# Optimization experiments

Measured on AMD Instinct MI355X. Metric: run time of the kernel, lower is better.

The kernel has to match this reference:

```python
import jax, jax.numpy as jnp
import numpy as np

D = 1024
H = 16
DH = D // H
L = 128  # max_pos_len
B = 4
T = 1024
SCALE = float(np.sqrt(D / H))


def setup_inputs() -> dict:
    key = jax.random.key(0)
    ks = jax.random.split(key, 9)
    x_q = jax.random.normal(ks[0], (B, T, D), dtype=jnp.float32)
    x_k = jax.random.normal(ks[1], (B, T, D), dtype=jnp.float32)
    x_v = jax.random.normal(ks[2], (B, T, D), dtype=jnp.float32)
    mask = jax.random.randint(ks[3], (B, 1, 1, T), 0, 2) == 1  # bool, True = masked
    Wq = jax.random.normal(ks[4], (D, D), dtype=jnp.float32) * 0.02
    Wk = jax.random.normal(ks[5], (D, D), dtype=jnp.float32) * 0.02
    Wv = jax.random.normal(ks[6], (D, D), dtype=jnp.float32) * 0.02
    Wo = jax.random.normal(ks[7], (D, D), dtype=jnp.float32) * 0.02
    pos_emb = jax.random.normal(ks[8], (2 * L + 1, DH), dtype=jnp.float32)
    return {"x_q": x_q, "x_k": x_k, "x_v": x_v, "mask": mask,
            "Wq": Wq, "Wk": Wk, "Wv": Wv, "Wo": Wo, "pos_emb": pos_emb}


def reference(x_q, x_k, x_v, mask, Wq, Wk, Wv, Wo, pos_emb):
    # nn.Linear(bias=False): y = x @ W.T
    def split_heads(x):  # (B,T,D) -> (B,H,T,DH)
        return x.reshape(B, -1, H, DH).transpose(0, 2, 1, 3)

    Q = split_heads(x_q @ Wq.T)
    K = split_heads(x_k @ Wk.T)
    V = split_heads(x_v @ Wv.T)

    logits = jnp.einsum('bhqd,bhkd->bhqk', Q, K)

    # arrange_char_pos_embedding: indices[q,k] = clamp(k-q, -L, L) + L
    rel = jnp.clip(jnp.arange(T)[None, :] - jnp.arange(T)[:, None], -L, L) + L
    arranged_pos = pos_emb[rel]  # (T_Q, T_K, DH)
    pos_logits = jnp.einsum('bhqd,qkd->bhqk', Q, arranged_pos)

    logits = (logits + pos_logits) / SCALE
    logits = jnp.where(mask, -jnp.inf, logits)  # mask broadcasts (B,1,1,T)
    attn = jax.nn.softmax(logits, axis=-1)  # dropout p=0.0 -> identity

    combined = jnp.einsum('bhqk,bhkd->bhqd', attn, V)
    heads_concat = combined.transpose(0, 2, 1, 3).reshape(B, -1, D)
    return heads_concat @ Wo.T
```

## Files before the change

kernel.cpp:

```cpp
#include <hip/hip_runtime.h>
#include <hip/hip_bf16.h>
#include <stdint.h>

typedef __attribute__((ext_vector_type(8))) short short8;
typedef __attribute__((ext_vector_type(4))) float f32x4;

__device__ __forceinline__ uint16_t f2bf(float f) {
    union { float f; uint32_t u; } v; v.f = f;
    uint32_t r = v.u + 0x7FFF + ((v.u >> 16) & 1);
    return (uint16_t)(r >> 16);
}
__device__ __forceinline__ float bf2f(uint16_t u) {
    union { uint32_t u; float f; } v; v.u = ((uint32_t)u) << 16;
    return v.f;
}
__device__ __forceinline__ float exp2_raw(float x) {
    float r;
    asm("v_exp_f32 %0, %1" : "=v"(r) : "v"(x));
    return r;
}
__device__ __forceinline__ uint32_t cvt_pk_bf16(float lo, float hi) {
    uint32_t r;
    asm("v_cvt_pk_bf16_f32 %0, %1, %2" : "=v"(r) : "v"(lo), "v"(hi));
    return r;
}

template<int F32>
__device__ __forceinline__ uint4 load8(const void* p, size_t off) {
    if (F32) {
        const float* f = (const float*)p + off;
        float4 f0 = *(const float4*)f;
        float4 f1 = *(const float4*)(f + 4);
        uint4 r;
        r.x = (uint32_t)f2bf(f0.x) | ((uint32_t)f2bf(f0.y) << 16);
        r.y = (uint32_t)f2bf(f0.z) | ((uint32_t)f2bf(f0.w) << 16);
        r.z = (uint32_t)f2bf(f1.x) | ((uint32_t)f2bf(f1.y) << 16);
        r.w = (uint32_t)f2bf(f1.z) | ((uint32_t)f2bf(f1.w) << 16);
        return r;
    } else {
        return *(const uint4*)((const uint16_t*)p + off);
    }
}

#define GLDS(gp, lp) __builtin_amdgcn_global_load_lds( \
    (const __attribute__((address_space(1))) void*)(gp), \
    (__attribute__((address_space(3))) void*)(lp), 16, 0, 0)

struct CvtSeg { const float* s; uint16_t* d; int n8; };
struct CvtArgs {
    CvtSeg seg[9]; int nseg;
    const void* mraw; unsigned long long* mbits; uint16_t* mvals;
};

__global__ __launch_bounds__(256) void cvt_bf16(CvtArgs a)
{
    if (blockIdx.x == 0) {
        __shared__ int flags[3];
        __shared__ uint8_t mloc[4096];
        const uint32_t* w = (const uint32_t*)a.mraw;
        const uint8_t* b8 = (const uint8_t*)a.mraw;
        const int t = threadIdx.x;
        if (t < 3) flags[t] = 0;
        __syncthreads();
        int fbyte = 0, ff32 = 0, fodd = 0;
        for (int i = t; i < 1024; i += 256) {
            uint32_t v = w[i];
            if (v != 0u && v != 1u && v != 0x3F800000u) fbyte = 1;
            if (v == 0x3F800000u) ff32 = 1;
            if ((i & 1) && v != 0u) fodd = 1;
        }
        if (fbyte) atomicOr(&flags[0], 1);
        if (ff32)  atomicOr(&flags[1], 1);
        if (fodd)  atomicOr(&flags[2], 1);
        __syncthreads();
        int mode;
        if (flags[0]) mode = 1;
        else if (flags[1]) mode = 0;
        else if (!flags[2]) mode = 2;
        else mode = 0;
        for (int k = t; k < 4096; k += 256) {
            int val;
            if (mode == 1)      val = (b8[k] != 0);
            else if (mode == 2) val = (w[2 * k] != 0u);
            else                val = (w[k] != 0u);
            mloc[k] = (uint8_t)val;
        }
        __syncthreads();
        for (int k = t; k < 4096; k += 256)
            a.mvals[k] = mloc[k] ? (uint16_t)0 : (uint16_t)0x3F80;
        if (t < 64) {
            uint64_t bits = 0;
#pragma unroll
            for (int i = 0; i < 64; ++i)
                bits |= (uint64_t)mloc[t * 64 + i] << i;
            a.mbits[t] = bits;
        }
    }
    const int tid = blockIdx.x * 256 + threadIdx.x;
    const int stride = gridDim.x * 256;
    for (int s = 0; s < a.nseg; ++s) {
        const float* src = a.seg[s].s;
        uint16_t* dst = a.seg[s].d;
        const int n8 = a.seg[s].n8;
        if (src) {
            for (int i = tid; i < n8; i += stride)
                *(uint4*)(dst + (size_t)i * 8) = load8<1>(src, (size_t)i * 8);
        } else {
            const uint4 z = {0u, 0u, 0u, 0u};
            for (int i = tid; i < n8; i += stride)
                *(uint4*)(dst + (size_t)i * 8) = z;
        }
    }
}

__global__ __launch_bounds__(256) void gemm128_qkv(
    const uint16_t* __restrict__ xq, const uint16_t* __restrict__ xk, const uint16_t* __restrict__ xv,
    const uint16_t* __restrict__ Wq, const uint16_t* __restrict__ Wk, const uint16_t* __restrict__ Wv,
    uint16_t* __restrict__ Qh, uint16_t* __restrict__ Khd, uint16_t* __restrict__ Vt,
    const unsigned long long* __restrict__ mbits)
{
    __shared__ alignas(16) uint16_t As[2][128 * 32];
    __shared__ alignas(16) uint16_t Bs[2][128 * 32];

    const int z = blockIdx.z;
    const uint16_t* A = (z == 0) ? xq : (z == 1) ? xk : xv;
    const uint16_t* B = (z == 0) ? Wq : (z == 1) ? Wk : Wv;
    uint16_t* C = (z == 0) ? Qh : (z == 1) ? Khd : Vt;
    const int cm = (z == 2) ? 2 : 1;
    const int bm = blockIdx.x, bn = blockIdx.y;
    const int K = 1024;

    const int t = threadIdx.x;
    const int lane = t & 63, wave = t >> 6;
    const int lrow = lane & 15, quad = lane >> 4;
    const int wr = (wave >> 1) * 64, wc = (wave & 1) * 64;
    const int g_row = wave * 16 + (lane >> 2);
    const int g_col = (lane & 3) * 8;

    const f32x4 fz = {0.f, 0.f, 0.f, 0.f};
    f32x4 acc[4][4];
#pragma unroll
    for (int i = 0; i < 4; ++i)
#pragma unroll
        for (int j = 0; j < 4; ++j) acc[i][j] = fz;

    for (int k0 = 0; k0 < K; k0 += 64) {
        __syncthreads();
#pragma unroll
        for (int kh = 0; kh < 2; ++kh) {
            const int kk = k0 + kh * 32;
            GLDS(A + (size_t)(bm * 128 + g_row) * K + kk + g_col,      As[kh] + wave * 512);
            GLDS(A + (size_t)(bm * 128 + g_row + 64) * K + kk + g_col, As[kh] + wave * 512 + 2048);
            GLDS(B + (size_t)(bn * 128 + g_row) * K + kk + g_col,      Bs[kh] + wave * 512);
            GLDS(B + (size_t)(bn * 128 + g_row + 64) * K + kk + g_col, Bs[kh] + wave * 512 + 2048);
        }
        __syncthreads();

#pragma unroll
        for (int kh = 0; kh < 2; ++kh) {
            short8 a[4], b[4];
#pragma unroll
            for (int i = 0; i < 4; ++i)
                a[i] = *(const short8*)(As[kh] + (wr + i * 16 + lrow) * 32 + quad * 8);
#pragma unroll
            for (int j = 0; j < 4; ++j)
                b[j] = *(const short8*)(Bs[kh] + (wc + j * 16 + lrow) * 32 + quad * 8);
#pragma unroll
            for (int i = 0; i < 4; ++i)
#pragma unroll
                for (int j = 0; j < 4; ++j)
                    acc[i][j] = __builtin_amdgcn_mfma_f32_16x16x32_bf16(a[i], b[j], acc[i][j], 0, 0, 0);
        }
    }

    if (cm == 2) {
        __syncthreads();
        uint16_t* scr = As[0] + wave * 1024;
        const int mg0 = bm * 128 + wr;
        const int widx = __builtin_amdgcn_readfirstlane((mg0 >> 10) * 16 + ((mg0 & 1023) >> 6));
        const uint64_t mword = mbits[widx];
        const uint64_t mw64 = mword >> ((lane & 1) * 8);
#pragma unroll
        for (int i = 0; i < 4; ++i)
#pragma unroll
            for (int j = 0; j < 4; ++j) {
                uint2 pk;
                pk.x = (uint32_t)f2bf(acc[i][j][0]) | ((uint32_t)f2bf(acc[i][j][1]) << 16);
                pk.y = (uint32_t)f2bf(acc[i][j][2]) | ((uint32_t)f2bf(acc[i][j][3]) << 16);
                *(uint2*)(scr + lrow * 16 + quad * 4) = pk;
                if (lane < 32) {
                    int n = lane >> 1, m8 = (lane & 1) * 8;
                    short8 vv = *(const short8*)(scr + n * 16 + m8);
                    int ng = bn * 128 + wc + j * 16 + n;
                    int hh = ng >> 6, d = ng & 63;
                    int mg = bm * 128 + wr + i * 16;
                    int bb = mg >> 10, tl = (mg & 1023) + m8;
                    uint32_t eb = (uint32_t)(mw64 >> (i * 16)) & 0xFFu;
                    if (eb) {
                        union { short8 s; uint32_t u[4]; } uw;
                        uw.s = vv;
#pragma unroll
                        for (int c = 0; c < 4; ++c) {
                            uint32_t km = (((eb >> (2 * c)) & 1) ? 0u : 0x0000FFFFu)
                                        | (((eb >> (2 * c + 1)) & 1) ? 0u : 0xFFFF0000u);
                            uw.u[c] &= km;
                        }
                        vv = uw.s;
                    }
                    *(short8*)(C + ((((size_t)bb * 16 + hh) * 64 + d) * 1024 + tl)) = vv;
                }
            }
        return;
    }

#pragma unroll
    for (int i = 0; i < 4; ++i)
#pragma unroll
        for (int j = 0; j < 4; ++j)
#pragma unroll
            for (int r = 0; r < 4; ++r) {
                int m = bm * 128 + wr + i * 16 + quad * 4 + r;
                int n = bn * 128 + wc + j * 16 + lrow;
                int bb = m >> 10, tt = m & 1023, hh = n >> 6, d = n & 63;
                C[(((size_t)bb * 16 + hh) * 1024 + tt) * 64 + d] = f2bf(acc[i][j][r]);
            }
}

__global__ __launch_bounds__(256) void gemm_out(
    const uint16_t* __restrict__ A, const uint16_t* __restrict__ B,
    float* __restrict__ C, int M, int N, int K)
{
    __shared__ alignas(16) uint16_t As[2][64 * 32];
    __shared__ alignas(16) uint16_t Bs[2][128 * 32];

    const int t = threadIdx.x;
    const int lane = t & 63, wave = t >> 6;
    const int lrow = lane & 15, quad = lane >> 4;
    const int wr = (wave >> 1) * 32, wc = (wave & 1) * 64;
    const int g_row = wave * 16 + (lane >> 2);
    const int g_col = (lane & 3) * 8;
    const int bm = blockIdx.x, bn = blockIdx.y;

    const f32x4 fz = {0.f, 0.f, 0.f, 0.f};
    f32x4 acc[2][4];
#pragma unroll
    for (int i = 0; i < 2; ++i)
#pragma unroll
        for (int j = 0; j < 4; ++j) acc[i][j] = fz;

    for (int k0 = 0; k0 < K; k0 += 64) {
        __syncthreads();
#pragma unroll
        for (int kh = 0; kh < 2; ++kh) {
            const int kk = k0 + kh * 32;
            GLDS(A + (size_t)(bm * 64 + g_row) * K + kk + g_col,       As[kh] + wave * 512);
            GLDS(B + (size_t)(bn * 128 + g_row) * K + kk + g_col,      Bs[kh] + wave * 512);
            GLDS(B + (size_t)(bn * 128 + g_row + 64) * K + kk + g_col, Bs[kh] + wave * 512 + 2048);
        }
        __syncthreads();

#pragma unroll
        for (int kh = 0; kh < 2; ++kh) {
            short8 a[2], b[4];
#pragma unroll
            for (int i = 0; i < 2; ++i)
                a[i] = *(const short8*)(As[kh] + (wr + i * 16 + lrow) * 32 + quad * 8);
#pragma unroll
            for (int j = 0; j < 4; ++j)
                b[j] = *(const short8*)(Bs[kh] + (wc + j * 16 + lrow) * 32 + quad * 8);
#pragma unroll
            for (int i = 0; i < 2; ++i)
#pragma unroll
                for (int j = 0; j < 4; ++j)
                    acc[i][j] = __builtin_amdgcn_mfma_f32_16x16x32_bf16(a[i], b[j], acc[i][j], 0, 0, 0);
        }
    }

#pragma unroll
    for (int i = 0; i < 2; ++i)
#pragma unroll
        for (int j = 0; j < 4; ++j)
#pragma unroll
            for (int r = 0; r < 4; ++r) {
                int m = bm * 64 + wr + i * 16 + quad * 4 + r;
                int n = bn * 128 + wc + j * 16 + lrow;
                C[(size_t)m * N + n] = acc[i][j][r];
            }
}

#define FA_QK(KC_)                                                              \
{                                                                               \
    _Pragma("unroll")                                                           \
    for (int j = 0; j < 4; ++j) {                                               \
        short8 k0 = *(const short8*)((KC_) + (j * 16 + lrow) * 32 + rdc);       \
        short8 k1 = *(const short8*)((KC_) + 2048 + (j * 16 + lrow) * 32 + rdc);\
        s[j] = __builtin_amdgcn_mfma_f32_16x16x32_bf16(aq0, k0, fz, 0, 0, 0);   \
        s[j] = __builtin_amdgcn_mfma_f32_16x16x32_bf16(aq1, k1, s[j], 0, 0, 0); \
    }                                                                           \
}

#define FA_PV(KBM_)                                                             \
{                                                                               \
    short8 bm0 = *(const short8*)(maskl + (KBM_) + quad * 8);                   \
    short8 bm1 = *(const short8*)(maskl + (KBM_) + 32 + quad * 8);              \
    _Pragma("unroll")                                                           \
    for (int dt = 0; dt < 4; ++dt) {                                            \
        o[dt] = __builtin_amdgcn_mfma_f32_16x16x32_bf16(ap0, vv[dt * 2 + 0], o[dt], 0, 0, 0); \
        o[dt] = __builtin_amdgcn_mfma_f32_16x16x32_bf16(ap1, vv[dt * 2 + 1], o[dt], 0, 0, 0); \
    }                                                                           \
    lacc = __builtin_amdgcn_mfma_f32_16x16x32_bf16(ap0, bm0, lacc, 0, 0, 0);    \
    lacc = __builtin_amdgcn_mfma_f32_16x16x32_bf16(ap1, bm1, lacc, 0, 0, 0);    \
}

#define FA_SM(KB_)                                                              \
{                                                                               \
    const int diff = (KB_) - qb;                                                \
    if (diff <= -192 || diff >= 144) {                                          \
        const bool low = (diff <= -192);                                        \
        _Pragma("unroll")                                                       \
        for (int j = 0; j < 4; ++j) {                                           \
            float e[4];                                                         \
            _Pragma("unroll")                                                   \
            for (int r = 0; r < 4; ++r) {                                       \
                float pc = low ? pcl[r] : pch[r];                               \
                e[r] = exp2_raw(__builtin_fmaf(s[j][r], CS, pc));               \
            }                                                                   \
            const uint32_t p01 = cvt_pk_bf16(e[0], e[1]);                       \
            const uint32_t p23 = cvt_pk_bf16(e[2], e[3]);                       \
            const int col = j * 16 + lrow;                                      \
            const int rw = quad * 4;                                            \
            Pl[wave][rw + 0][col] = (uint16_t)p01;                              \
            Pl[wave][rw + 1][col] = (uint16_t)(p01 >> 16);                      \
            Pl[wave][rw + 2][col] = (uint16_t)p23;                              \
            Pl[wave][rw + 3][col] = (uint16_t)(p23 >> 16);                      \
        }                                                                       \
    } else {                                                                    \
        _Pragma("unroll")                                                       \
        for (int j = 0; j < 4; ++j) {                                           \
            const int key = (KB_) + j * 16 + lrow;                              \
            float e[4];                                                         \
            _Pragma("unroll")                                                   \
            for (int r = 0; r < 4; ++r) {                                       \
                int q = qb + quad * 4 + r;                                      \
                int ql = q & 63;                                                \
                int rel = min(max(key - q, -128), 128) + 128;                   \
                float p = bf2f(Qpos_l[ql][rel]);                                \
                e[r] = exp2_raw(__builtin_fmaf(s[j][r], CS, p));                \
            }                                                                   \
            const uint32_t p01 = cvt_pk_bf16(e[0], e[1]);                       \
            const uint32_t p23 = cvt_pk_bf16(e[2], e[3]);                       \
            const int col = j * 16 + lrow;                                      \
            const int rw = quad * 4;                                            \
            Pl[wave][rw + 0][col] = (uint16_t)p01;                              \
            Pl[wave][rw + 1][col] = (uint16_t)(p01 >> 16);                      \
            Pl[wave][rw + 2][col] = (uint16_t)p23;                              \
            Pl[wave][rw + 3][col] = (uint16_t)(p23 >> 16);                      \
        }                                                                       \
    }                                                                           \
    ap0 = *(const short8*)(&Pl[wave][lrow][quad * 8]);                          \
    ap1 = *(const short8*)(&Pl[wave][lrow][32 + quad * 8]);                     \
}

#define FA_VV(VC_)                                                              \
{                                                                               \
    _Pragma("unroll")                                                           \
    for (int dt = 0; dt < 4; ++dt) {                                            \
        vv[dt * 2 + 0] = *(const short8*)((VC_) + (dt * 16 + lrow) * 32 + rdc); \
        vv[dt * 2 + 1] = *(const short8*)((VC_) + 2048 + (dt * 16 + lrow) * 32 + rdc); \
    }                                                                           \
}

__global__ __launch_bounds__(256) void flash_attn(
    const uint16_t* __restrict__ Qh, const uint16_t* __restrict__ Kh,
    const uint16_t* __restrict__ Vt, const uint16_t* __restrict__ pos,
    const uint16_t* __restrict__ maskv, uint16_t* __restrict__ comb)
{
    const int blk = blockIdx.x;
    const int jj = blk >> 3;
    const int bh = (blk & 7) * 8 + (jj >> 4);
    const int qt = jj & 15;
    const int b = bh >> 4;
    const int h = bh & 15;
    const int t = threadIdx.x;
    const int lane = t & 63;
    const int wave = t >> 6;
    const int lrow = lane & 15;
    const int quad = lane >> 4;
    const int qb = qt * 64 + wave * 16;

    __shared__ alignas(16) uint16_t Ks[2][4096];
    __shared__ alignas(16) uint16_t Vs[2][4096];
    __shared__ alignas(16) uint16_t Qpos_l[64][277];
    __shared__ alignas(16) uint16_t Pl[4][16][72];
    __shared__ alignas(16) uint16_t maskl[1024];

    const uint16_t* Kp = Kh + (size_t)bh * 65536;
    const uint16_t* Vp = Vt + (size_t)bh * 65536;

    const int sg_r = lane >> 2;
    const int sg_c = ((lane & 3) ^ ((sg_r >> 1) & 3)) * 8;
    const int hw = wave >> 1;
    const int gw = (wave & 1) * 2;
    const int rdc = (quad ^ ((lrow >> 1) & 3)) * 8;

    const float CS = 0.18033688011f;

#pragma unroll
    for (int gg = 0; gg < 2; ++gg) {
        int g = gw + gg;
        GLDS(Kp + (size_t)(g * 16 + sg_r) * 64 + hw * 32 + sg_c, &Ks[0][hw * 2048 + g * 512]);
        GLDS(Vp + (size_t)(g * 16 + sg_r) * 1024 + hw * 32 + sg_c, &Vs[0][hw * 2048 + g * 512]);
    }
    if (wave < 2)
        GLDS(maskv + (size_t)b * 1024 + wave * 512 + lane * 8, maskl + wave * 512);

    const uint16_t* Qp = Qh + ((size_t)bh * 1024 + qb) * 64;
    short8 aq0 = *(const short8*)(Qp + (size_t)lrow * 64 + quad * 8);
    short8 aq1 = *(const short8*)(Qp + (size_t)lrow * 64 + 32 + quad * 8);

    const f32x4 fz = {0.f, 0.f, 0.f, 0.f};

#pragma unroll 4
    for (int nt = 0; nt < 17; ++nt) {
        short8 pb0 = *(const short8*)(pos + (size_t)(nt * 16 + lrow) * 64 + quad * 8);
        short8 pb1 = *(const short8*)(pos + (size_t)(nt * 16 + lrow) * 64 + 32 + quad * 8);
        f32x4 c = __builtin_amdgcn_mfma_f32_16x16x32_bf16(aq0, pb0, fz, 0, 0, 0);
        c = __builtin_amdgcn_mfma_f32_16x16x32_bf16(aq1, pb1, c, 0, 0, 0);
        const uint32_t p01 = cvt_pk_bf16(c[0] * CS, c[1] * CS);
        const uint32_t p23 = cvt_pk_bf16(c[2] * CS, c[3] * CS);
        const int row = wave * 16 + quad * 4;
        const int col = nt * 16 + lrow;
        Qpos_l[row + 0][col] = (uint16_t)p01;
        Qpos_l[row + 1][col] = (uint16_t)(p01 >> 16);
        Qpos_l[row + 2][col] = (uint16_t)p23;
        Qpos_l[row + 3][col] = (uint16_t)(p23 >> 16);
    }

    float pcl[4], pch[4];
#pragma unroll
    for (int r = 0; r < 4; ++r) {
        int ql = wave * 16 + quad * 4 + r;
        pcl[r] = bf2f(Qpos_l[ql][0]);
        pch[r] = bf2f(Qpos_l[ql][256]);
    }

    f32x4 o[4] = {fz, fz, fz, fz};
    f32x4 lacc = fz;
    f32x4 s[4];
    short8 ap0, ap1, vv[8];

    __syncthreads();
#pragma unroll
    for (int gg = 0; gg < 2; ++gg) {
        int g = gw + gg;
        GLDS(Kp + (size_t)(64 + g * 16 + sg_r) * 64 + hw * 32 + sg_c, &Ks[1][hw * 2048 + g * 512]);
        GLDS(Vp + (size_t)(g * 16 + sg_r) * 1024 + 64 + hw * 32 + sg_c, &Vs[1][hw * 2048 + g * 512]);
    }
    __builtin_amdgcn_s_setprio(1);
    FA_QK(Ks[0])
    __builtin_amdgcn_s_setprio(0);
    FA_SM(0)
    FA_VV(Vs[0])

    for (int ti = 1; ti < 16; ++ti) {
        const int kb = ti * 64;
        const uint16_t* Kc = Ks[ti & 1];
        const uint16_t* Vc = Vs[ti & 1];
        __syncthreads();
        if (ti < 15) {
            const int nxt = (ti + 1) & 1;
#pragma unroll
            for (int gg = 0; gg < 2; ++gg) {
                int g = gw + gg;
                GLDS(Kp + (size_t)(kb + 64 + g * 16 + sg_r) * 64 + hw * 32 + sg_c,
                     &Ks[nxt][hw * 2048 + g * 512]);
                GLDS(Vp + (size_t)(g * 16 + sg_r) * 1024 + kb + 64 + hw * 32 + sg_c,
                     &Vs[nxt][hw * 2048 + g * 512]);
            }
        }
        __builtin_amdgcn_s_setprio(1);
        FA_PV(kb - 64)
        FA_QK(Kc)
        __builtin_amdgcn_s_setprio(0);
        FA_SM(kb)
        FA_VV(Vc)
    }
    __builtin_amdgcn_s_setprio(1);
    FA_PV(960)
    __builtin_amdgcn_s_setprio(0);

    float inv[4];
#pragma unroll
    for (int r = 0; r < 4; ++r) inv[r] = 1.0f / lacc[r];

#pragma unroll
    for (int dt = 0; dt < 4; ++dt)
#pragma unroll
        for (int r = 0; r < 4; ++r) {
            size_t row = (size_t)b * 1024 + qb + quad * 4 + r;
            size_t col = (size_t)h * 64 + dt * 16 + lrow;
            comb[row * 1024 + col] = f2bf(o[dt][r] * inv[r]);
        }
}

extern "C" void kernel_launch(void* const* d_in, const int* in_sizes, int n_in,
                              void* d_out, int out_size, void* d_ws, size_t ws_size,
                              hipStream_t stream)
{
    const float* x_q = (const float*)d_in[0];
    const float* x_k = (const float*)d_in[1];
    const float* x_v = (const float*)d_in[2];
    const void*  msk = d_in[3];
    const float* Wq  = (const float*)d_in[4];
    const float* Wk  = (const float*)d_in[5];
    const float* Wv  = (const float*)d_in[6];
    const float* Wo  = (const float*)d_in[7];
    const float* pos = (const float*)d_in[8];

    char* ws = (char*)d_ws;
    const size_t MB = 1u << 20;
    uint16_t* Qh   = (uint16_t*)(ws);
    uint16_t* Khd  = (uint16_t*)(ws + 8 * MB);
    uint16_t* Vt   = (uint16_t*)(ws + 16 * MB);
    uint16_t* xqb  = (uint16_t*)(ws + 24 * MB);
    uint16_t* xkb  = (uint16_t*)(ws + 32 * MB);
    uint16_t* xvb  = (uint16_t*)(ws + 40 * MB);
    uint16_t* Wqb  = (uint16_t*)(ws + 48 * MB);
    uint16_t* Wkb  = (uint16_t*)(ws + 50 * MB);
    uint16_t* Wvb  = (uint16_t*)(ws + 52 * MB);
    uint16_t* Wob  = (uint16_t*)(ws + 54 * MB);
    uint16_t* posb = (uint16_t*)(ws + 56 * MB);
    unsigned long long* mbits = (unsigned long long*)(ws + 56 * MB + 65536);
    uint16_t* mvals = (uint16_t*)(ws + 56 * MB + 65536 + 4096);
    uint16_t* comb = xqb;

    CvtArgs ca{};
    int ns = 0;
    ca.seg[ns++] = {x_q, xqb, 524288};
    ca.seg[ns++] = {x_k, xkb, 524288};
    ca.seg[ns++] = {x_v, xvb, 524288};
    ca.seg[ns++] = {Wq, Wqb, 131072};
    ca.seg[ns++] = {Wk, Wkb, 131072};
    ca.seg[ns++] = {Wv, Wvb, 131072};
    ca.seg[ns++] = {Wo, Wob, 131072};
    ca.seg[ns++] = {pos, posb, 2056};
    ca.seg[ns++] = {nullptr, posb + 16448, 120};
    ca.nseg = ns;
    ca.mraw = msk;
    ca.mbits = mbits;
    ca.mvals = mvals;
    cvt_bf16<<<dim3(512), dim3(256), 0, stream>>>(ca);

    gemm128_qkv<<<dim3(32, 8, 3), dim3(256), 0, stream>>>(
        xqb, xkb, xvb, Wqb, Wkb, Wvb, Qh, Khd, Vt, mbits);

    flash_attn<<<dim3(1024), dim3(256), 0, stream>>>(Qh, Khd, Vt, posb, mvals, comb);

    gemm_out<<<dim3(64, 8), dim3(256), 0, stream>>>(
        comb, Wob, (float*)d_out, 4096, 1024, 1024);
}
```

Baseline: 229.2 us.

## Store K/V in MFMA fragment order and load directly to registers

```diff
diff --git a/kernel.cpp b/kernel.cpp
--- a/kernel.cpp
+++ b/kernel.cpp
@@ -207,7 +207,11 @@
                         }
                         vv = uw.s;
                     }
-                    *(short8*)(C + ((((size_t)bb * 16 + hh) * 64 + d) * 1024 + tl)) = vv;
+                    size_t addr = (size_t)(bb * 16 + hh) * 65536
+                                + (size_t)((tl >> 6) * 4096
+                                           + ((d >> 4) * 2 + ((tl >> 5) & 1)) * 512
+                                           + ((tl >> 3) & 3) * 128 + (d & 15) * 8);
+                    *(short8*)(C + addr) = vv;
                 }
             }
         return;
@@ -221,8 +225,16 @@
             for (int r = 0; r < 4; ++r) {
                 int m = bm * 128 + wr + i * 16 + quad * 4 + r;
                 int n = bn * 128 + wc + j * 16 + lrow;
-                int bb = m >> 10, tt = m & 1023, hh = n >> 6, d = n & 63;
-                C[(((size_t)bb * 16 + hh) * 1024 + tt) * 64 + d] = f2bf(acc[i][j][r]);
+                int bb = m >> 10, key = m & 1023, hh = n >> 6, d = n & 63;
+                if (z == 0) {
+                    C[(((size_t)bb * 16 + hh) * 1024 + key) * 64 + d] = f2bf(acc[i][j][r]);
+                } else {
+                    size_t addr = (size_t)(bb * 16 + hh) * 65536
+                                + (size_t)((key >> 6) * 4096
+                                           + (((key >> 4) & 3) * 2 + (d >> 5)) * 512
+                                           + ((d >> 3) & 3) * 128 + (key & 15) * 8 + (d & 7));
+                    C[addr] = f2bf(acc[i][j][r]);
+                }
             }
 }
 
@@ -286,30 +298,6 @@
                 int n = bn * 128 + wc + j * 16 + lrow;
                 C[(size_t)m * N + n] = acc[i][j][r];
             }
-}
-
-#define FA_QK(KC_)                                                              \
-{                                                                               \
-    _Pragma("unroll")                                                           \
-    for (int j = 0; j < 4; ++j) {                                               \
-        short8 k0 = *(const short8*)((KC_) + (j * 16 + lrow) * 32 + rdc);       \
-        short8 k1 = *(const short8*)((KC_) + 2048 + (j * 16 + lrow) * 32 + rdc);\
-        s[j] = __builtin_amdgcn_mfma_f32_16x16x32_bf16(aq0, k0, fz, 0, 0, 0);   \
-        s[j] = __builtin_amdgcn_mfma_f32_16x16x32_bf16(aq1, k1, s[j], 0, 0, 0); \
-    }                                                                           \
-}
-
-#define FA_PV(KBM_)                                                             \
-{                                                                               \
-    short8 bm0 = *(const short8*)(maskl + (KBM_) + quad * 8);                   \
-    short8 bm1 = *(const short8*)(maskl + (KBM_) + 32 + quad * 8);              \
-    _Pragma("unroll")                                                           \
-    for (int dt = 0; dt < 4; ++dt) {                                            \
-        o[dt] = __builtin_amdgcn_mfma_f32_16x16x32_bf16(ap0, vv[dt * 2 + 0], o[dt], 0, 0, 0); \
-        o[dt] = __builtin_amdgcn_mfma_f32_16x16x32_bf16(ap1, vv[dt * 2 + 1], o[dt], 0, 0, 0); \
-    }                                                                           \
-    lacc = __builtin_amdgcn_mfma_f32_16x16x32_bf16(ap0, bm0, lacc, 0, 0, 0);    \
-    lacc = __builtin_amdgcn_mfma_f32_16x16x32_bf16(ap1, bm1, lacc, 0, 0, 0);    \
 }
 
 #define FA_SM(KB_)                                                              \
@@ -361,13 +349,41 @@
     ap1 = *(const short8*)(&Pl[wave][lrow][32 + quad * 8]);                     \
 }
 
-#define FA_VV(VC_)                                                              \
+#define FA_BODY(TI, KC, KN, MC, MN)                                             \
 {                                                                               \
+    const int kb = (TI) * 64;                                                   \
+                      \
+    const uint16_t* vb = Vp + (size_t)(TI) * 4096;                              \
+    short8 vv[8];                                                               \
+    _Pragma("unroll")                                                           \
+    for (int sl = 0; sl < 8; ++sl)                                              \
+        vv[sl] = *(const short8*)(vb + sl * 512 + lane8);                       \
+                                               \
+    const int tn = ((TI) + 1) & 15;                                             \
+    const uint16_t* kbn = Kp + (size_t)tn * 4096;                               \
+    _Pragma("unroll")                                                           \
+    for (int sl = 0; sl < 8; ++sl)                                              \
+        KN[sl] = *(const short8*)(kbn + sl * 512 + lane8);                      \
+    MN[0] = *(const short8*)(mkb + tn * 64 + quad * 8);                         \
+    MN[1] = *(const short8*)(mkb + tn * 64 + 32 + quad * 8);                    \
+    f32x4 s[4];                                                                 \
+    __builtin_amdgcn_s_setprio(1);                                              \
+    _Pragma("unroll")                                                           \
+    for (int j = 0; j < 4; ++j) {                                               \
+        s[j] = __builtin_amdgcn_mfma_f32_16x16x32_bf16(aq0, KC[j * 2 + 0], fz, 0, 0, 0); \
+        s[j] = __builtin_amdgcn_mfma_f32_16x16x32_bf16(aq1, KC[j * 2 + 1], s[j], 0, 0, 0); \
+    }                                                                           \
+    __builtin_amdgcn_s_setprio(0);                                              \
+    FA_SM(kb)                                                                   \
+    __builtin_amdgcn_s_setprio(1);                                              \
     _Pragma("unroll")                                                           \
     for (int dt = 0; dt < 4; ++dt) {                                            \
-        vv[dt * 2 + 0] = *(const short8*)((VC_) + (dt * 16 + lrow) * 32 + rdc); \
-        vv[dt * 2 + 1] = *(const short8*)((VC_) + 2048 + (dt * 16 + lrow) * 32 + rdc); \
+        o[dt] = __builtin_amdgcn_mfma_f32_16x16x32_bf16(ap0, vv[dt * 2 + 0], o[dt], 0, 0, 0); \
+        o[dt] = __builtin_amdgcn_mfma_f32_16x16x32_bf16(ap1, vv[dt * 2 + 1], o[dt], 0, 0, 0); \
     }                                                                           \
+    lacc = __builtin_amdgcn_mfma_f32_16x16x32_bf16(ap0, MC[0], lacc, 0, 0, 0);  \
+    lacc = __builtin_amdgcn_mfma_f32_16x16x32_bf16(ap1, MC[1], lacc, 0, 0, 0);  \
+    __builtin_amdgcn_s_setprio(0);                                              \
 }
 
 __global__ __launch_bounds__(256) void flash_attn(
@@ -387,32 +403,23 @@
     const int lrow = lane & 15;
     const int quad = lane >> 4;
     const int qb = qt * 64 + wave * 16;
-
-    __shared__ alignas(16) uint16_t Ks[2][4096];
-    __shared__ alignas(16) uint16_t Vs[2][4096];
+    const int lane8 = lane * 8;
+
     __shared__ alignas(16) uint16_t Qpos_l[64][277];
     __shared__ alignas(16) uint16_t Pl[4][16][72];
-    __shared__ alignas(16) uint16_t maskl[1024];
 
     const uint16_t* Kp = Kh + (size_t)bh * 65536;
     const uint16_t* Vp = Vt + (size_t)bh * 65536;
-
-    const int sg_r = lane >> 2;
-    const int sg_c = ((lane & 3) ^ ((sg_r >> 1) & 3)) * 8;
-    const int hw = wave >> 1;
-    const int gw = (wave & 1) * 2;
-    const int rdc = (quad ^ ((lrow >> 1) & 3)) * 8;
+    const uint16_t* mkb = maskv + (size_t)b * 1024;
 
     const float CS = 0.18033688011f;
 
-#pragma unroll
-    for (int gg = 0; gg < 2; ++gg) {
-        int g = gw + gg;
-        GLDS(Kp + (size_t)(g * 16 + sg_r) * 64 + hw * 32 + sg_c, &Ks[0][hw * 2048 + g * 512]);
-        GLDS(Vp + (size_t)(g * 16 + sg_r) * 1024 + hw * 32 + sg_c, &Vs[0][hw * 2048 + g * 512]);
-    }
-    if (wave < 2)
-        GLDS(maskv + (size_t)b * 1024 + wave * 512 + lane * 8, maskl + wave * 512);
+    short8 ka[8], kn[8], ma[2], mn[2];
+#pragma unroll
+    for (int sl = 0; sl < 8; ++sl)
+        ka[sl] = *(const short8*)(Kp + sl * 512 + lane8);
+    ma[0] = *(const short8*)(mkb + quad * 8);
+    ma[1] = *(const short8*)(mkb + 32 + quad * 8);
 
     const uint16_t* Qp = Qh + ((size_t)bh * 1024 + qb) * 64;
     short8 aq0 = *(const short8*)(Qp + (size_t)lrow * 64 + quad * 8);
@@ -446,48 +453,12 @@
 
     f32x4 o[4] = {fz, fz, fz, fz};
     f32x4 lacc = fz;
-    f32x4 s[4];
-    short8 ap0, ap1, vv[8];
-
-    __syncthreads();
-#pragma unroll
-    for (int gg = 0; gg < 2; ++gg) {
-        int g = gw + gg;
-        GLDS(Kp + (size_t)(64 + g * 16 + sg_r) * 64 + hw * 32 + sg_c, &Ks[1][hw * 2048 + g * 512]);
-        GLDS(Vp + (size_t)(g * 16 + sg_r) * 1024 + 64 + hw * 32 + sg_c, &Vs[1][hw * 2048 + g * 512]);
-    }
-    __builtin_amdgcn_s_setprio(1);
-    FA_QK(Ks[0])
-    __builtin_amdgcn_s_setprio(0);
-    FA_SM(0)
-    FA_VV(Vs[0])
-
-    for (int ti = 1; ti < 16; ++ti) {
-        const int kb = ti * 64;
-        const uint16_t* Kc = Ks[ti & 1];
-        const uint16_t* Vc = Vs[ti & 1];
-        __syncthreads();
-        if (ti < 15) {
-            const int nxt = (ti + 1) & 1;
-#pragma unroll
-            for (int gg = 0; gg < 2; ++gg) {
-                int g = gw + gg;
-                GLDS(Kp + (size_t)(kb + 64 + g * 16 + sg_r) * 64 + hw * 32 + sg_c,
-                     &Ks[nxt][hw * 2048 + g * 512]);
-                GLDS(Vp + (size_t)(g * 16 + sg_r) * 1024 + kb + 64 + hw * 32 + sg_c,
-                     &Vs[nxt][hw * 2048 + g * 512]);
-            }
-        }
-        __builtin_amdgcn_s_setprio(1);
-        FA_PV(kb - 64)
-        FA_QK(Kc)
-        __builtin_amdgcn_s_setprio(0);
-        FA_SM(kb)
-        FA_VV(Vc)
-    }
-    __builtin_amdgcn_s_setprio(1);
-    FA_PV(960)
-    __builtin_amdgcn_s_setprio(0);
+    short8 ap0, ap1;
+
+    for (int t2 = 0; t2 < 16; t2 += 2) {
+        FA_BODY(t2, ka, kn, ma, mn)
+        FA_BODY(t2 + 1, kn, ka, mn, ma)
+    }
 
     float inv[4];
 #pragma unroll
```

After: 245.5 us. +7.1%, slower.

## Store V in MFMA fragment order and load it directly from global memory

Applied to the files above, without the earlier changes.

```diff
diff --git a/kernel.cpp b/kernel.cpp
--- a/kernel.cpp
+++ b/kernel.cpp
@@ -207,7 +207,11 @@
                         }
                         vv = uw.s;
                     }
-                    *(short8*)(C + ((((size_t)bb * 16 + hh) * 64 + d) * 1024 + tl)) = vv;
+                    size_t addr = (size_t)(bb * 16 + hh) * 65536
+                                + (size_t)((tl >> 6) * 4096
+                                           + ((d >> 4) * 2 + ((tl >> 5) & 1)) * 512
+                                           + ((tl >> 3) & 3) * 128 + (d & 15) * 8);
+                    *(short8*)(C + addr) = vv;
                 }
             }
         return;
@@ -286,30 +290,6 @@
                 int n = bn * 128 + wc + j * 16 + lrow;
                 C[(size_t)m * N + n] = acc[i][j][r];
             }
-}
-
-#define FA_QK(KC_)                                                              \
-{                                                                               \
-    _Pragma("unroll")                                                           \
-    for (int j = 0; j < 4; ++j) {                                               \
-        short8 k0 = *(const short8*)((KC_) + (j * 16 + lrow) * 32 + rdc);       \
-        short8 k1 = *(const short8*)((KC_) + 2048 + (j * 16 + lrow) * 32 + rdc);\
-        s[j] = __builtin_amdgcn_mfma_f32_16x16x32_bf16(aq0, k0, fz, 0, 0, 0);   \
-        s[j] = __builtin_amdgcn_mfma_f32_16x16x32_bf16(aq1, k1, s[j], 0, 0, 0); \
-    }                                                                           \
-}
-
-#define FA_PV(KBM_)                                                             \
-{                                                                               \
-    short8 bm0 = *(const short8*)(maskl + (KBM_) + quad * 8);                   \
-    short8 bm1 = *(const short8*)(maskl + (KBM_) + 32 + quad * 8);              \
-    _Pragma("unroll")                                                           \
-    for (int dt = 0; dt < 4; ++dt) {                                            \
-        o[dt] = __builtin_amdgcn_mfma_f32_16x16x32_bf16(ap0, vv[dt * 2 + 0], o[dt], 0, 0, 0); \
-        o[dt] = __builtin_amdgcn_mfma_f32_16x16x32_bf16(ap1, vv[dt * 2 + 1], o[dt], 0, 0, 0); \
-    }                                                                           \
-    lacc = __builtin_amdgcn_mfma_f32_16x16x32_bf16(ap0, bm0, lacc, 0, 0, 0);    \
-    lacc = __builtin_amdgcn_mfma_f32_16x16x32_bf16(ap1, bm1, lacc, 0, 0, 0);    \
 }
 
 #define FA_SM(KB_)                                                              \
@@ -361,16 +341,7 @@
     ap1 = *(const short8*)(&Pl[wave][lrow][32 + quad * 8]);                     \
 }
 
-#define FA_VV(VC_)                                                              \
-{                                                                               \
-    _Pragma("unroll")                                                           \
-    for (int dt = 0; dt < 4; ++dt) {                                            \
-        vv[dt * 2 + 0] = *(const short8*)((VC_) + (dt * 16 + lrow) * 32 + rdc); \
-        vv[dt * 2 + 1] = *(const short8*)((VC_) + 2048 + (dt * 16 + lrow) * 32 + rdc); \
-    }                                                                           \
-}
-
-__global__ __launch_bounds__(256) void flash_attn(
+__global__ __launch_bounds__(256, 3) void flash_attn(
     const uint16_t* __restrict__ Qh, const uint16_t* __restrict__ Kh,
     const uint16_t* __restrict__ Vt, const uint16_t* __restrict__ pos,
     const uint16_t* __restrict__ maskv, uint16_t* __restrict__ comb)
@@ -387,15 +358,15 @@
     const int lrow = lane & 15;
     const int quad = lane >> 4;
     const int qb = qt * 64 + wave * 16;
-
-    __shared__ alignas(16) uint16_t Ks[2][4096];
-    __shared__ alignas(16) uint16_t Vs[2][4096];
+    const int lane8 = lane * 8;
+
+    __shared__ alignas(16) uint16_t Ks[4096];
     __shared__ alignas(16) uint16_t Qpos_l[64][277];
     __shared__ alignas(16) uint16_t Pl[4][16][72];
-    __shared__ alignas(16) uint16_t maskl[1024];
 
     const uint16_t* Kp = Kh + (size_t)bh * 65536;
     const uint16_t* Vp = Vt + (size_t)bh * 65536;
+    const uint16_t* mkb = maskv + (size_t)b * 1024;
 
     const int sg_r = lane >> 2;
     const int sg_c = ((lane & 3) ^ ((sg_r >> 1) & 3)) * 8;
@@ -408,11 +379,8 @@
 #pragma unroll
     for (int gg = 0; gg < 2; ++gg) {
         int g = gw + gg;
-        GLDS(Kp + (size_t)(g * 16 + sg_r) * 64 + hw * 32 + sg_c, &Ks[0][hw * 2048 + g * 512]);
-        GLDS(Vp + (size_t)(g * 16 + sg_r) * 1024 + hw * 32 + sg_c, &Vs[0][hw * 2048 + g * 512]);
-    }
-    if (wave < 2)
-        GLDS(maskv + (size_t)b * 1024 + wave * 512 + lane * 8, maskl + wave * 512);
+        GLDS(Kp + (size_t)(g * 16 + sg_r) * 64 + hw * 32 + sg_c, &Ks[hw * 2048 + g * 512]);
+    }
 
     const uint16_t* Qp = Qh + ((size_t)bh * 1024 + qb) * 64;
     short8 aq0 = *(const short8*)(Qp + (size_t)lrow * 64 + quad * 8);
@@ -446,48 +414,55 @@
 
     f32x4 o[4] = {fz, fz, fz, fz};
     f32x4 lacc = fz;
-    f32x4 s[4];
-    short8 ap0, ap1, vv[8];
-
-    __syncthreads();
-#pragma unroll
-    for (int gg = 0; gg < 2; ++gg) {
-        int g = gw + gg;
-        GLDS(Kp + (size_t)(64 + g * 16 + sg_r) * 64 + hw * 32 + sg_c, &Ks[1][hw * 2048 + g * 512]);
-        GLDS(Vp + (size_t)(g * 16 + sg_r) * 1024 + 64 + hw * 32 + sg_c, &Vs[1][hw * 2048 + g * 512]);
-    }
-    __builtin_amdgcn_s_setprio(1);
-    FA_QK(Ks[0])
-    __builtin_amdgcn_s_setprio(0);
-    FA_SM(0)
-    FA_VV(Vs[0])
-
-    for (int ti = 1; ti < 16; ++ti) {
+    short8 ap0, ap1;
+
+    for (int ti = 0; ti < 16; ++ti) {
         const int kb = ti * 64;
-        const uint16_t* Kc = Ks[ti & 1];
-        const uint16_t* Vc = Vs[ti & 1];
+        __syncthreads();
+        short8 kr[8];
+#pragma unroll
+        for (int j = 0; j < 4; ++j) {
+            kr[j * 2 + 0] = *(const short8*)(Ks + (j * 16 + lrow) * 32 + rdc);
+            kr[j * 2 + 1] = *(const short8*)(Ks + 2048 + (j * 16 + lrow) * 32 + rdc);
+        }
         __syncthreads();
         if (ti < 15) {
-            const int nxt = (ti + 1) & 1;
 #pragma unroll
             for (int gg = 0; gg < 2; ++gg) {
                 int g = gw + gg;
                 GLDS(Kp + (size_t)(kb + 64 + g * 16 + sg_r) * 64 + hw * 32 + sg_c,
-                     &Ks[nxt][hw * 2048 + g * 512]);
-                GLDS(Vp + (size_t)(g * 16 + sg_r) * 1024 + kb + 64 + hw * 32 + sg_c,
-                     &Vs[nxt][hw * 2048 + g * 512]);
+                     &Ks[hw * 2048 + g * 512]);
             }
         }
+        const uint16_t* vb = Vp + (size_t)ti * 4096;
+        short8 vv[8];
+#pragma unroll
+        for (int sl = 0; sl < 8; ++sl)
+            vv[sl] = *(const short8*)(vb + sl * 512 + lane8);
+        short8 bm0 = *(const short8*)(mkb + kb + quad * 8);
+        short8 bm1 = *(const short8*)(mkb + kb + 32 + quad * 8);
+
+        f32x4 s[4];
         __builtin_amdgcn_s_setprio(1);
-        FA_PV(kb - 64)
-        FA_QK(Kc)
+#pragma unroll
+        for (int j = 0; j < 4; ++j) {
+            s[j] = __builtin_amdgcn_mfma_f32_16x16x32_bf16(aq0, kr[j * 2 + 0], fz, 0, 0, 0);
+            s[j] = __builtin_amdgcn_mfma_f32_16x16x32_bf16(aq1, kr[j * 2 + 1], s[j], 0, 0, 0);
+        }
         __builtin_amdgcn_s_setprio(0);
+
         FA_SM(kb)
-        FA_VV(Vc)
-    }
-    __builtin_amdgcn_s_setprio(1);
-    FA_PV(960)
-    __builtin_amdgcn_s_setprio(0);
+
+        __builtin_amdgcn_s_setprio(1);
+#pragma unroll
+        for (int dt = 0; dt < 4; ++dt) {
+            o[dt] = __builtin_amdgcn_mfma_f32_16x16x32_bf16(ap0, vv[dt * 2 + 0], o[dt], 0, 0, 0);
+            o[dt] = __builtin_amdgcn_mfma_f32_16x16x32_bf16(ap1, vv[dt * 2 + 1], o[dt], 0, 0, 0);
+        }
+        lacc = __builtin_amdgcn_mfma_f32_16x16x32_bf16(ap0, bm0, lacc, 0, 0, 0);
+        lacc = __builtin_amdgcn_mfma_f32_16x16x32_bf16(ap1, bm1, lacc, 0, 0, 0);
+        __builtin_amdgcn_s_setprio(0);
+    }
 
     float inv[4];
 #pragma unroll
```

Result: faster. 224.1 us (-2.2%).
